# Kernel tuning notes

Measured on AMD Instinct MI355X. Metric: run time of the kernel, lower is better.

Reference implementation:

```python
import jax, jax.numpy as jnp
import numpy as np

B, CIN, COUT, SDIM, RES, K = 8, 512, 512, 512, 64, 3
AFF_SCALE = 1.0 / np.sqrt(SDIM)          # LinearAct: 1/sqrt(in_features)
CONV_SCALE = 1.0 / np.sqrt(CIN * K * K)  # ModulatedConv2d: 1/sqrt(in*k*k)
LRELU_GAIN = np.sqrt(2.0)                # bias_act 'lrelu' default gain


def setup_inputs() -> dict:
    key = jax.random.key(0)
    k = jax.random.split(key, 5)
    x = jax.random.normal(k[0], (B, CIN, RES, RES), dtype=jnp.float32)
    w = jax.random.normal(k[1], (B, SDIM), dtype=jnp.float32)
    noise = jax.random.normal(k[2], (B, 1, RES, RES), dtype=jnp.float32)
    affine_w = jax.random.normal(k[3], (CIN, SDIM), dtype=jnp.float32)
    affine_b = jnp.ones((CIN,), dtype=jnp.float32)          # bias.data.fill_(1.0)
    conv_w = jax.random.normal(k[4], (COUT, CIN, K, K), dtype=jnp.float32)
    noise_scale = jnp.asarray(0.1, dtype=jnp.float32)        # InjectNoise.scale (nonzero for a meaningful test)
    bias = jnp.zeros((COUT,), dtype=jnp.float32)
    return {"x": x, "w": w, "noise": noise, "affine_w": affine_w,
            "affine_b": affine_b, "conv_w": conv_w,
            "noise_scale": noise_scale, "bias": bias}


def reference(x, w, noise, affine_w, affine_b, conv_w, noise_scale, bias):
    # affine (LinearAct, act='linear'): style = w @ (W*scale)^T + b
    style = jnp.einsum('bs,cs->bc', w, affine_w * AFF_SCALE) + affine_b  # [B, CIN]

    # modulate + demodulate: per-sample weight [B, COUT, CIN, K, K]
    wt = conv_w[None] * style[:, None, :, None, None] * CONV_SCALE
    d = jax.lax.rsqrt(jnp.sum(wt * wt, axis=(2, 3, 4), keepdims=True) + 1e-8)
    wt = wt * d

    # grouped conv (groups=B) == per-sample conv; flip_weight=True -> plain correlation
    def conv_one(xi, wi):
        return jax.lax.conv_general_dilated(
            xi[None], wi, window_strides=(1, 1), padding=[(1, 1), (1, 1)],
            dimension_numbers=('NCHW', 'OIHW', 'NCHW'))[0]

    y = jax.vmap(conv_one)(x, wt)  # [B, COUT, RES, RES]

    # noise -> bias -> lrelu(0.2) * sqrt(2)
    y = y + noise * noise_scale
    y = jax.nn.leaky_relu(y + bias[None, :, None, None], 0.2) * LRELU_GAIN
    return y
```

## Files before the change

kernel.cpp:

```cpp
#include <hip/hip_runtime.h>
#include <hip/hip_bf16.h>

typedef unsigned short u16;

#define BATCH 8
#define CIN 512
#define COUT 512
#define SDIM 512
#define RES 64
#define PIX (RES * RES)
#define NKT 72
#define PPIX 4356
#define PANEL_E 139392

__device__ __constant__ static const float kAffScale  = 0.04419417382415922f;
__device__ __constant__ static const float kConvScale = 0.014731391274719742f;
__device__ __constant__ static const float kGain      = 1.4142135623730951f;

typedef __bf16 bf16x8 __attribute__((ext_vector_type(8)));
typedef float  f32x4  __attribute__((ext_vector_type(4)));

__global__ void style_k(const float* __restrict__ w, const float* __restrict__ aw,
                        const float* __restrict__ ab, float* __restrict__ style) {
  int tid = blockIdx.x * 256 + threadIdx.x;
  int b = tid >> 9, c = tid & 511;
  const float* wp = w + b * SDIM;
  const float* ap = aw + c * SDIM;
  float s = 0.0f;
  for (int k = 0; k < SDIM; ++k) s += wp[k] * ap[k];
  style[tid] = s * kAffScale + ab[c];
}

__global__ void cw2_k(const float* __restrict__ cw, float* __restrict__ cw2) {
  int tid = blockIdx.x * 256 + threadIdx.x;
  const float* p = cw + tid * 9;
  float s = 0.0f;
  #pragma unroll
  for (int t = 0; t < 9; ++t) { float v = p[t]; s += v * v; }
  cw2[tid] = s;
}

__global__ void fac_k(const float* __restrict__ style, const float* __restrict__ cw2,
                      float* __restrict__ fac) {
  int wid  = blockIdx.x * 4 + (threadIdx.x >> 6);
  int lane = threadIdx.x & 63;
  int b = wid >> 9, o = wid & 511;
  const float* st = style + b * CIN;
  const float* c2 = cw2 + o * CIN;
  float s = 0.0f;
  for (int i = lane; i < CIN; i += 64) { float sv = st[i]; s += sv * sv * c2[i]; }
  #pragma unroll
  for (int off = 32; off; off >>= 1) s += __shfl_xor(s, off);
  if (lane == 0) {
    float d = rsqrtf(s * kConvScale * kConvScale + 1e-8f);
    fac[wid] = d * kConvScale;
  }
}

__global__ void wcast_k(const float* __restrict__ cw, u16* __restrict__ wbt) {
  int tid = blockIdx.x * 256 + threadIdx.x;
  int o = tid >> 9, i = tid & 511;
  const float* p = cw + tid * 9;
  #pragma unroll
  for (int t = 0; t < 9; ++t) {
    __hip_bfloat16 h = __float2bfloat16(p[t]);
    wbt[((size_t)(t * 16 + (i >> 5)) * 512 + o) * 32 + (i & 31)] = *(u16*)&h;
  }
}

__global__ void bz_k(u16* __restrict__ xst) {
  int idx = blockIdx.x * 256 + threadIdx.x;
  if (idx >= 128 * PPIX) return;
  int pan = idx / PPIX, pix = idx - pan * PPIX;
  int h = pix / 66, w = pix - h * 66;
  if (h == 0 || h == 65 || w == 0 || w == 65) {
    u16* p = xst + (size_t)pan * PANEL_E + (size_t)pix * 32;
    int4 z = make_int4(0, 0, 0, 0);
    ((int4*)p)[0] = z; ((int4*)p)[1] = z; ((int4*)p)[2] = z; ((int4*)p)[3] = z;
  }
}

__global__ void modx_k(const float* __restrict__ x, const float* __restrict__ style,
                       u16* __restrict__ xst) {
  __shared__ float t[64][65];
  int b  = blockIdx.z;
  int it = blockIdx.y * 64;
  int pt = blockIdx.x * 64;
  int tp = threadIdx.x & 63;
  int tr = threadIdx.x >> 6;
  for (int r = tr; r < 64; r += 4) {
    int i = it + r;
    t[r][tp] = x[(b * CIN + i) * PIX + pt + tp] * style[b * CIN + i];
  }
  __syncthreads();
  int i = it + tp;
  size_t pbase = (size_t)(b * 16 + (i >> 5)) * PANEL_E + (i & 31);
  for (int r = tr; r < 64; r += 4) {
    int pix = pt + r, h = pix >> 6, w = pix & 63;
    __hip_bfloat16 hh = __float2bfloat16(t[tp][r]);
    xst[pbase + (size_t)((h + 1) * 66 + (w + 1)) * 32] = *(u16*)&hh;
  }
}

__launch_bounds__(512, 2)
__global__ void gemm_k(const u16* __restrict__ wbt, const u16* __restrict__ xst,
                       const float* __restrict__ fac, const float* __restrict__ noise,
                       const float* __restrict__ nscale_p, const float* __restrict__ bias,
                       float* __restrict__ y) {
  __shared__ __align__(16) u16 Abuf[2][16384];
  __shared__ __align__(16) u16 Bbuf[2][16384];

  const int tid = threadIdx.x;
  const int bid = blockIdx.x;
  const int swz = (bid & 7) * 32 + (bid >> 3);
  const int mt = swz >> 7;
  const int nt = swz & 127;
  const int b  = nt >> 4;
  const int pimg  = (nt & 15) * 256;
  const int hbase = pimg >> 6;

  const int lane = tid & 63;
  const int wv = tid >> 6;
  const int wm = wv >> 2;
  const int wn = wv & 3;
  const int l15 = lane & 15, l4 = lane >> 4;
  const int slot = (l4 ^ ((l15 >> 1) & 3)) * 8;

  const int sgE = ((tid & 3) ^ ((tid >> 3) & 3)) << 3;
  int aoffE[2], ppB[2];
  #pragma unroll
  for (int p = 0; p < 2; ++p) {
    int row = (p * 512 + tid) >> 2;
    aoffE[p] = (mt * 256 + row) * 32 + sgE;
    ppB[p]   = ((hbase + (row >> 6) + 1) * 66 + (row & 63) + 1) * 32 + sgE;
  }

  auto stA = [&](int ktx, int kh) {
    if (ktx >= NKT) ktx -= NKT;
    const int d = ktx & 1;
    const u16* pan = wbt + ((size_t)(2 * ktx + kh) << 14);
    #pragma unroll
    for (int p = 0; p < 2; ++p) {
      __builtin_amdgcn_global_load_lds(
          (const __attribute__((address_space(1))) void*)(pan + aoffE[p]),
          (__attribute__((address_space(3))) void*)(&Abuf[d][kh * 8192 + (p * 512 + tid) * 8]),
          16, 0, 0);
    }
  };
  auto stB = [&](int ktx, int kh) {
    if (ktx >= NKT) ktx -= NKT;
    const int tap = ktx >> 3;
    const int t3  = (tap >= 6) ? 2 : (tap >= 3 ? 1 : 0);
    const int shiftE = ((t3 - 1) * 66 + (tap - t3 * 3 - 1)) * 32;
    const int d = ktx & 1;
    const u16* pan = xst + (size_t)(b * 16 + ((ktx & 7) << 1) + kh) * PANEL_E + shiftE;
    #pragma unroll
    for (int p = 0; p < 2; ++p) {
      __builtin_amdgcn_global_load_lds(
          (const __attribute__((address_space(1))) void*)(pan + ppB[p]),
          (__attribute__((address_space(3))) void*)(&Bbuf[d][kh * 8192 + (p * 512 + tid) * 8]),
          16, 0, 0);
    }
  };

  f32x4 acc[8][4];
  #pragma unroll
  for (int i = 0; i < 8; ++i)
    #pragma unroll
    for (int j = 0; j < 4; ++j) acc[i][j] = (f32x4){0.f, 0.f, 0.f, 0.f};

  stA(0, 0); stB(0, 0); stA(0, 1); stB(0, 1); stA(1, 0); stB(1, 0);
  asm volatile("s_waitcnt vmcnt(8)" ::: "memory");
  __builtin_amdgcn_s_barrier();

#define LDA(D, mi, kh) (*(const bf16x8*)&Abuf[D][(kh) * 8192 + (wm * 128 + (mi) * 16 + l15) * 32 + slot])
#define LDB(D, ni, kh) (*(const bf16x8*)&Bbuf[D][(kh) * 8192 + (wn * 64 + (ni) * 16 + l15) * 32 + slot])

#define HALF(D, KT, KH, STKT, STKH) {                                          \
    bf16x8 bfr[4], af[4], afp[4];                                              \
    _Pragma("unroll") for (int ni = 0; ni < 4; ++ni) bfr[ni] = LDB(D, ni, KH); \
    _Pragma("unroll") for (int j = 0; j < 4; ++j) af[j] = LDA(D, j, KH);       \
    __builtin_amdgcn_sched_barrier(0);   \
    _Pragma("unroll") for (int j = 0; j < 4; ++j) afp[j] = LDA(D, 4 + j, KH);  \
    stA(STKT, STKH);                                                           \
    __builtin_amdgcn_s_barrier();                                              \
    asm volatile("s_waitcnt lgkmcnt(4)" ::: "memory");                         \
    __builtin_amdgcn_sched_barrier(0);                                         \
    __builtin_amdgcn_s_setprio(1);                                             \
    _Pragma("unroll") for (int j = 0; j < 4; ++j)                              \
      _Pragma("unroll") for (int ni = 0; ni < 4; ++ni)                         \
        acc[j][ni] = __builtin_amdgcn_mfma_f32_16x16x32_bf16(af[j], bfr[ni], acc[j][ni], 0, 0, 0); \
    __builtin_amdgcn_s_setprio(0);                                             \
    __builtin_amdgcn_s_barrier();                                              \
    stB(STKT, STKH);                                                           \
    asm volatile("s_waitcnt lgkmcnt(0)" ::: "memory");                         \
    __builtin_amdgcn_sched_barrier(0);                                         \
    __builtin_amdgcn_s_setprio(1);                                             \
    _Pragma("unroll") for (int j = 0; j < 4; ++j)                              \
      _Pragma("unroll") for (int ni = 0; ni < 4; ++ni)                         \
        acc[4 + j][ni] = __builtin_amdgcn_mfma_f32_16x16x32_bf16(afp[j], bfr[ni], acc[4 + j][ni], 0, 0, 0); \
    __builtin_amdgcn_s_setprio(0);                                             \
    asm volatile("s_waitcnt vmcnt(8)" ::: "memory");                           \
    __builtin_amdgcn_s_barrier();                                              \
  }

  for (int kt = 0; kt < NKT; kt += 2) {
    HALF(0, kt, 0, kt + 1, 1)
    HALF(0, kt, 1, kt + 2, 0)
    HALF(1, kt + 1, 0, kt + 2, 1)
    HALF(1, kt + 1, 1, kt + 3, 0)
  }
#undef HALF
#undef LDA
#undef LDB

  const float ns = nscale_p[0];
  float nz[4];
  #pragma unroll
  for (int ni = 0; ni < 4; ++ni) {
    int pix = pimg + wn * 64 + ni * 16 + l15;
    nz[ni] = noise[b * PIX + pix] * ns;
  }
  #pragma unroll
  for (int mi = 0; mi < 8; ++mi) {
    int o = mt * 256 + wm * 128 + mi * 16 + l4 * 4;
    f32x4 fv = *(const f32x4*)&fac[b * COUT + o];
    f32x4 bv = *(const f32x4*)&bias[o];
    #pragma unroll
    for (int r = 0; r < 4; ++r) {
      float* yp = y + (size_t)(b * COUT + o + r) * PIX + pimg + wn * 64 + l15;
      #pragma unroll
      for (int ni = 0; ni < 4; ++ni) {
        float v = acc[mi][ni][r] * fv[r] + nz[ni] + bv[r];
        v = (v > 0.0f ? v : 0.2f * v) * kGain;
        yp[ni * 16] = v;
      }
    }
  }
}

extern "C" void kernel_launch(void* const* d_in, const int* in_sizes, int n_in,
                              void* d_out, int out_size, void* d_ws, size_t ws_size,
                              hipStream_t stream) {
  const float* x      = (const float*)d_in[0];
  const float* w      = (const float*)d_in[1];
  const float* noise  = (const float*)d_in[2];
  const float* aff_w  = (const float*)d_in[3];
  const float* aff_b  = (const float*)d_in[4];
  const float* conv_w = (const float*)d_in[5];
  const float* nscale = (const float*)d_in[6];
  const float* bias   = (const float*)d_in[7];
  float* y = (float*)d_out;

  char* ws = (char*)d_ws;
  float* style = (float*)(ws);
  float* fac   = (float*)(ws + 16384);
  float* cw2   = (float*)(ws + 32768);
  u16*   wbt   = (u16*)(ws + 1081600);
  u16*   xst   = (u16*)(ws + 5800192);

  style_k<<<16, 256, 0, stream>>>(w, aff_w, aff_b, style);
  cw2_k<<<1024, 256, 0, stream>>>(conv_w, cw2);
  fac_k<<<1024, 256, 0, stream>>>(style, cw2, fac);
  wcast_k<<<1024, 256, 0, stream>>>(conv_w, wbt);
  bz_k<<<(128 * PPIX + 255) / 256, 256, 0, stream>>>(xst);
  modx_k<<<dim3(64, 8, 8), 256, 0, stream>>>(x, style, xst);
  gemm_k<<<256, 512, 0, stream>>>(wbt, xst, fac, noise, nscale, bias, y);
}
```

Before: 198.8 us.

## Stage input halo tile once per channel block and reuse across all nine taps

Instead of loading a shifted B tile from global memory for each of the nine conv taps, the kernel loads a haloed input patch (rows plus borders) into LDS once per 64-channel block and reads tap-shifted windows from it. The loop is reordered from tap-major to channel-block-major, and the A weights now use a 3-slot ring buffer. This is meant to cut global/L2 traffic for the activation operand roughly ninefold. In exchange LDS use grows to about 147KB, which may reduce occupancy below two blocks per CU, and the halo load adds bigger vmcnt waits at block boundaries.

```diff
diff --git a/kernel.cpp b/kernel.cpp
--- a/kernel.cpp
+++ b/kernel.cpp
@@ -9,7 +9,6 @@
 #define SDIM 512
 #define RES 64
 #define PIX (RES * RES)
-#define NKT 72
 #define PPIX 4356
 #define PANEL_E 139392
 
@@ -107,8 +106,7 @@
                        const float* __restrict__ fac, const float* __restrict__ noise,
                        const float* __restrict__ nscale_p, const float* __restrict__ bias,
                        float* __restrict__ y) {
-  __shared__ __align__(16) u16 Abuf[2][16384];
-  __shared__ __align__(16) u16 Bbuf[2][16384];
+  __shared__ __align__(16) u16 lds[75264];
 
   const int tid = threadIdx.x;
   const int bid = blockIdx.x;
@@ -124,42 +122,55 @@
   const int wm = wv >> 2;
   const int wn = wv & 3;
   const int l15 = lane & 15, l4 = lane >> 4;
-  const int slot = (l4 ^ ((l15 >> 1) & 3)) * 8;
+  const int pwn = (wn + 1) * 66 + l15;
+
+  int aElem[8];
+  #pragma unroll
+  for (int mi = 0; mi < 8; ++mi) {
+    int arow = wm * 128 + mi * 16 + l15;
+    aElem[mi] = arow * 32 + ((l4 ^ ((arow >> 1) & 3)) << 3);
+  }
 
   const int sgE = ((tid & 3) ^ ((tid >> 3) & 3)) << 3;
-  int aoffE[2], ppB[2];
-  #pragma unroll
-  for (int p = 0; p < 2; ++p) {
-    int row = (p * 512 + tid) >> 2;
-    aoffE[p] = (mt * 256 + row) * 32 + sgE;
-    ppB[p]   = ((hbase + (row >> 6) + 1) * 66 + (row & 63) + 1) * 32 + sgE;
-  }
-
-  auto stA = [&](int ktx, int kh) {
-    if (ktx >= NKT) ktx -= NKT;
-    const int d = ktx & 1;
-    const u16* pan = wbt + ((size_t)(2 * ktx + kh) << 14);
+  int aoffE[2];
+  #pragma unroll
+  for (int p = 0; p < 2; ++p)
+    aoffE[p] = (mt * 256 + ((p * 512 + tid) >> 2)) * 32 + sgE;
+
+  auto stA = [&](int panel, int ring) {
+    const u16* pan = wbt + ((size_t)panel << 14);
     #pragma unroll
     for (int p = 0; p < 2; ++p) {
       __builtin_amdgcn_global_load_lds(
           (const __attribute__((address_space(1))) void*)(pan + aoffE[p]),
-          (__attribute__((address_space(3))) void*)(&Abuf[d][kh * 8192 + (p * 512 + tid) * 8]),
+          (__attribute__((address_space(3))) void*)(&lds[ring * 8192 + (p * 512 + tid) * 8]),
           16, 0, 0);
     }
   };
-  auto stB = [&](int ktx, int kh) {
-    if (ktx >= NKT) ktx -= NKT;
-    const int tap = ktx >> 3;
-    const int t3  = (tap >= 6) ? 2 : (tap >= 3 ? 1 : 0);
-    const int shiftE = ((t3 - 1) * 66 + (tap - t3 * 3 - 1)) * 32;
-    const int d = ktx & 1;
-    const u16* pan = xst + (size_t)(b * 16 + ((ktx & 7) << 1) + kh) * PANEL_E + shiftE;
-    #pragma unroll
-    for (int p = 0; p < 2; ++p) {
+
+  auto stHalo = [&](int cbn) {
+    const int dst0 = 24576 + (cbn & 1) * 25344;
+    const size_t srcPan = (size_t)(b * 16 + cbn * 2) * PANEL_E + (size_t)(hbase * 66) * 32;
+    #pragma unroll
+    for (int pass = 0; pass < 6; ++pass) {
+      int c = pass * 512 + tid;
+      int kh = c >= 1584 ? 1 : 0;
+      int r = c - (kh ? 1584 : 0);
+      int p = r >> 2;
+      int sg = (c & 3) ^ ((p >> 1) & 3);
+      const u16* src = xst + srcPan + (size_t)kh * PANEL_E + p * 32 + sg * 8;
       __builtin_amdgcn_global_load_lds(
-          (const __attribute__((address_space(1))) void*)(pan + ppB[p]),
-          (__attribute__((address_space(3))) void*)(&Bbuf[d][kh * 8192 + (p * 512 + tid) * 8]),
-          16, 0, 0);
+          (const __attribute__((address_space(1))) void*)src,
+          (__attribute__((address_space(3))) void*)(&lds[dst0 + c * 8]), 16, 0, 0);
+    }
+    if (tid < 96) {
+      int c = 3072 + tid;
+      int p = (c - 1584) >> 2;
+      int sg = (c & 3) ^ ((p >> 1) & 3);
+      const u16* src = xst + srcPan + (size_t)PANEL_E + p * 32 + sg * 8;
+      __builtin_amdgcn_global_load_lds(
+          (const __attribute__((address_space(1))) void*)src,
+          (__attribute__((address_space(3))) void*)(&lds[dst0 + c * 8]), 16, 0, 0);
     }
   };
 
@@ -169,50 +180,62 @@
     #pragma unroll
     for (int j = 0; j < 4; ++j) acc[i][j] = (f32x4){0.f, 0.f, 0.f, 0.f};
 
-  stA(0, 0); stB(0, 0); stA(0, 1); stB(0, 1); stA(1, 0); stB(1, 0);
-  asm volatile("s_waitcnt vmcnt(8)" ::: "memory");
+  stHalo(0);
+  stA(0, 0);
+  stA(1, 1);
+  asm volatile("s_waitcnt vmcnt(2)" ::: "memory");
   __builtin_amdgcn_s_barrier();
 
-#define LDA(D, mi, kh) (*(const bf16x8*)&Abuf[D][(kh) * 8192 + (wm * 128 + (mi) * 16 + l15) * 32 + slot])
-#define LDB(D, ni, kh) (*(const bf16x8*)&Bbuf[D][(kh) * 8192 + (wn * 64 + (ni) * 16 + l15) * 32 + slot])
-
-#define HALF(D, KT, KH, STKT, STKH) {                                          \
-    bf16x8 bfr[4], af[4], afp[4];                                              \
-    _Pragma("unroll") for (int ni = 0; ni < 4; ++ni) bfr[ni] = LDB(D, ni, KH); \
-    _Pragma("unroll") for (int j = 0; j < 4; ++j) af[j] = LDA(D, j, KH);       \
-    __builtin_amdgcn_sched_barrier(0);   \
-    _Pragma("unroll") for (int j = 0; j < 4; ++j) afp[j] = LDA(D, 4 + j, KH);  \
-    stA(STKT, STKH);                                                           \
+#define PH(IDX) {                                                              \
+    constexpr int tap_ = (IDX) >> 1, kh_ = (IDX) & 1;                          \
+    constexpr int rr_ = (IDX) % 3;                                             \
+    constexpr int nI_ = (IDX) + 2;                                             \
+    constexpr int tapS_ = (nI_ % 18) >> 1, khS_ = (nI_ % 18) & 1;              \
+    constexpr int rw_ = nI_ % 3;                                               \
+    constexpr int dy_ = tap_ / 3 - 1, dx_ = tap_ % 3 - 1;                      \
+    const int sb_ = 24576 + (cb & 1) * 25344 + kh_ * 12672;                    \
+    bf16x8 bfr[4], af03[4], af47[4];                                           \
+    _Pragma("unroll") for (int ni = 0; ni < 4; ++ni) {                         \
+      int prow = pwn + (dy_ * 66 + dx_ + 1 + ni * 16);                         \
+      int sl = (l4 ^ ((prow >> 1) & 3)) << 3;                                  \
+      bfr[ni] = *(const bf16x8*)&lds[sb_ + prow * 32 + sl];                    \
+    }                                                                          \
+    _Pragma("unroll") for (int j = 0; j < 4; ++j)                              \
+      af03[j] = *(const bf16x8*)&lds[rr_ * 8192 + aElem[j]];                   \
+    __builtin_amdgcn_sched_barrier(0);    \
+    _Pragma("unroll") for (int j = 0; j < 4; ++j)                              \
+      af47[j] = *(const bf16x8*)&lds[rr_ * 8192 + aElem[4 + j]];               \
+    stA(tapS_ * 16 + khS_ + ((nI_ >= 18) ? cbw : cb) * 2, rw_);                \
+    if ((IDX) == 15) stHalo(cbw);                                              \
     __builtin_amdgcn_s_barrier();                                              \
     asm volatile("s_waitcnt lgkmcnt(4)" ::: "memory");                         \
     __builtin_amdgcn_sched_barrier(0);                                         \
     __builtin_amdgcn_s_setprio(1);                                             \
     _Pragma("unroll") for (int j = 0; j < 4; ++j)                              \
       _Pragma("unroll") for (int ni = 0; ni < 4; ++ni)                         \
-        acc[j][ni] = __builtin_amdgcn_mfma_f32_16x16x32_bf16(af[j], bfr[ni], acc[j][ni], 0, 0, 0); \
+        acc[j][ni] = __builtin_amdgcn_mfma_f32_16x16x32_bf16(af03[j], bfr[ni], acc[j][ni], 0, 0, 0); \
     __builtin_amdgcn_s_setprio(0);                                             \
-    __builtin_amdgcn_s_barrier();                                              \
-    stB(STKT, STKH);                                                           \
     asm volatile("s_waitcnt lgkmcnt(0)" ::: "memory");                         \
     __builtin_amdgcn_sched_barrier(0);                                         \
     __builtin_amdgcn_s_setprio(1);                                             \
     _Pragma("unroll") for (int j = 0; j < 4; ++j)                              \
       _Pragma("unroll") for (int ni = 0; ni < 4; ++ni)                         \
-        acc[4 + j][ni] = __builtin_amdgcn_mfma_f32_16x16x32_bf16(afp[j], bfr[ni], acc[4 + j][ni], 0, 0, 0); \
+        acc[4 + j][ni] = __builtin_amdgcn_mfma_f32_16x16x32_bf16(af47[j], bfr[ni], acc[4 + j][ni], 0, 0, 0); \
     __builtin_amdgcn_s_setprio(0);                                             \
-    asm volatile("s_waitcnt vmcnt(8)" ::: "memory");                           \
+    if ((IDX) == 15 || (IDX) == 16) {                                          \
+      asm volatile("s_waitcnt vmcnt(8)" ::: "memory");                         \
+    } else {                                                                   \
+      asm volatile("s_waitcnt vmcnt(2)" ::: "memory");                         \
+    }                                                                          \
     __builtin_amdgcn_s_barrier();                                              \
   }
 
-  for (int kt = 0; kt < NKT; kt += 2) {
-    HALF(0, kt, 0, kt + 1, 1)
-    HALF(0, kt, 1, kt + 2, 0)
-    HALF(1, kt + 1, 0, kt + 2, 1)
-    HALF(1, kt + 1, 1, kt + 3, 0)
-  }
-#undef HALF
-#undef LDA
-#undef LDB
+  for (int cb = 0; cb < 8; ++cb) {
+    const int cbw = (cb == 7) ? 0 : cb + 1;
+    PH(0)  PH(1)  PH(2)  PH(3)  PH(4)  PH(5)  PH(6)  PH(7)  PH(8)
+    PH(9)  PH(10) PH(11) PH(12) PH(13) PH(14) PH(15) PH(16) PH(17)
+  }
+#undef PH
 
   const float ns = nscale_p[0];
   float nz[4];
```

Result: faster. 191.5 us (-3.7%).
